# Performance work log

Measured on AMD Instinct MI355X. Metric: run time of the kernel, lower is better.

Reference implementation:

```python
import jax, jax.numpy as jnp
import numpy as np

N, F, H, T = 8192, 64, 64, 64   # nodes, fea_hid, gcn_hid, trans_hid
E = 262144                       # edges (avg degree 32)
S, K = 128, 128                  # subgraphs, subgraph size
NEG = 4                          # neg_num


def prelu(x, a):
    return jnp.where(x >= 0, x, a * x)


def setup_inputs() -> dict:
    key = jax.random.key(0)
    ks = jax.random.split(key, 20)
    inp = {}
    inp["feat"] = jax.random.normal(ks[0], (N, F), jnp.float32)
    inp["edge_src"] = jax.random.randint(ks[1], (E,), 0, N)
    inp["edge_dst"] = jax.random.randint(ks[2], (E,), 0, N)
    inp["edge_w"] = jax.random.uniform(ks[3], (E,), jnp.float32)   # normalized adj values
    inp["avg_w"] = jax.random.uniform(ks[4], (E,), jnp.float32)    # adj_avg values
    inp["neg_idx1"] = jax.random.randint(ks[5], (NEG, N), 0, N)
    inp["neg_idx2"] = jax.random.randint(ks[6], (NEG, N), 0, N)
    inp["a_subg_idx"] = jax.random.randint(ks[7], (S, K), 0, N)
    inp["n_subg_idx"] = jax.random.randint(ks[8], (S, K), 0, N)
    inp["a_lap"] = jax.random.normal(ks[9], (S, K, K), jnp.float32) * 0.1
    inp["n_lap"] = jax.random.normal(ks[10], (S, K, K), jnp.float32) * 0.1
    sc = lambda k, sh, d: jax.random.normal(k, sh, jnp.float32) / np.float32(np.sqrt(d))
    inp["W1"] = sc(ks[11], (F, H), F); inp["b1"] = jnp.zeros((H,), jnp.float32)
    inp["W2"] = sc(ks[12], (H, H), H); inp["b2"] = jnp.zeros((H,), jnp.float32)
    inp["Wq"] = sc(ks[13], (H, T), H); inp["bq"] = jnp.zeros((T,), jnp.float32)
    inp["Ws"] = sc(ks[14], (T, 1), T); inp["bs"] = jnp.zeros((1,), jnp.float32)
    inp["B1"] = sc(ks[15], (F, T), F); inp["bd1"] = jnp.zeros((), jnp.float32)
    inp["B2"] = sc(ks[16], (T, H), T); inp["bd2"] = jnp.zeros((), jnp.float32)
    inp["a1"] = jnp.full((), 0.25, jnp.float32)  # PReLU slopes
    inp["a2"] = jnp.full((), 0.25, jnp.float32)
    inp["aq"] = jnp.full((), 0.25, jnp.float32)
    return inp


def _agg(h, src, dst, w):
    # sparse matmul: (sparse adj) @ h via gather + segment_sum
    return jax.ops.segment_sum(w[:, None] * h[src], dst, num_segments=N)


def _forward(feat, edge_w, avg_w, a_lap, n_lap, W1, b1, W2, b2, Wq, bq, Ws, bs,
             B1, bd1, B2, bd2, a1, a2, aq,
             edge_src, edge_dst, neg_idx1, neg_idx2, a_subg_idx, n_subg_idx):
    # GCN 1: fc -> spmm -> +bias -> PReLU ; node_transemb = pre-propagation features
    h1 = feat @ W1                                             # [N,H]  node_transemb
    v1 = prelu(_agg(h1, edge_src, edge_dst, edge_w) + b1, a1)  # [N,H]
    # GCN 2
    h2 = v1 @ W2
    v2 = prelu(_agg(h2, edge_src, edge_dst, edge_w) + b2, a2)
    # transq + PReLU
    node_vec = prelu(v2 @ Wq + bq, aq)                          # [N,T]
    # AvgNeighbor on node_transemb
    node_neighbor = _agg(h1, edge_src, edge_dst, avg_w)         # [N,H]
    # Discriminator 1: bilinear(feat, node_vec); negatives shuffle feat
    p1 = jnp.einsum('nf,ft,nt->n', feat, B1, node_vec) + bd1    # [N]
    n1 = jnp.einsum('knf,ft,nt->kn', feat[neg_idx1], B1, node_vec) + bd1  # [NEG,N]
    # Discriminator 2: bilinear(node_vec, node_neighbor); negatives shuffle node_vec
    p2 = jnp.einsum('nt,th,nh->n', node_vec, B2, node_neighbor) + bd2
    n2 = jnp.einsum('knt,th,nh->kn', node_vec[neg_idx2], B2, node_neighbor) + bd2
    # MIL scores
    score = jax.nn.sigmoid(node_vec @ Ws + bs)[:, 0]            # [N]
    # batched subgraph losses (replaces ragged python loop)
    a_s = score[a_subg_idx]                                     # [S,K]
    n_s = score[n_subg_idx]                                     # [S,K]
    hom = (jnp.einsum('sk,skj,sj->s', a_s, a_lap, a_s)
           + jnp.einsum('sk,skj,sj->s', n_s, n_lap, n_s))       # [S]
    a_sort = -jnp.sort(-a_s, axis=1)                            # descending sort
    n_sort = -jnp.sort(-n_s, axis=1)
    # first position with value below the subgraph mean
    avg_idx = jnp.argmax(a_sort < jnp.mean(a_sort, axis=1, keepdims=True), axis=1)  # [S]
    a_at_avg = jnp.take_along_axis(a_sort, avg_idx[:, None], axis=1)[:, 0]
    ranking_loss = jnp.mean(jax.nn.relu(1.0 - a_sort[:, 0] + n_sort[:, 0]))
    ranking_inner_loss = jnp.mean(jax.nn.relu(1.0 - a_sort[:, 0] + a_at_avg))
    sp_loss = jnp.mean(jnp.sum(a_s, axis=1))
    hom_loss = jnp.sum(hom) / (2.0 * S)
    adj_rebuilt = jax.nn.sigmoid(node_vec @ node_vec.T)         # [N,N]
    return (ranking_loss, ranking_inner_loss, sp_loss, hom_loss, adj_rebuilt,
            p1, n1, p2, n2)


def reference(feat, edge_src, edge_dst, edge_w, avg_w, neg_idx1, neg_idx2,
              a_subg_idx, n_subg_idx, a_lap, n_lap,
              W1, b1, W2, b2, Wq, bq, Ws, bs, B1, bd1, B2, bd2, a1, a2, aq):
    return _forward(feat, edge_w, avg_w, a_lap, n_lap, W1, b1, W2, b2, Wq, bq, Ws, bs,
                    B1, bd1, B2, bd2, a1, a2, aq,
                    edge_src, edge_dst, neg_idx1, neg_idx2, a_subg_idx, n_subg_idx)
```

## Files before the change

### kernel.cpp

```cpp
#include <hip/hip_runtime.h>

#define Nn 8192
#define Ee 262144
#define NEGk 4

#define OFF_H1   0u
#define OFF_M1   524288u
#define OFF_V1   1048576u
#define OFF_NN   1572864u
#define OFF_H2   2097152u
#define OFF_V2   2621440u
#define OFF_NV   3145728u
#define OFF_M2   3670016u
#define OFF_SC   4194304u
#define OFF_CNT  4203008u
#define OFF_CUR  4211200u
#define OFF_RS   4219392u
#define OFF_ESRC 4227600u
#define OFF_EW   4489744u
#define OFF_EAW  4751888u
#define OFF_NVH  5014032u
#define OFF_NVL  5276176u
#define OFF_WT   5538320u

using short8 = __attribute__((ext_vector_type(8))) short;
using f32x4  = __attribute__((ext_vector_type(4))) float;

__device__ inline float wave_sum(float v){
  #pragma unroll
  for (int o = 32; o > 0; o >>= 1) v += __shfl_down(v, o, 64);
  return v;
}
__device__ inline float wave_max(float v){
  #pragma unroll
  for (int o = 32; o > 0; o >>= 1) v = fmaxf(v, __shfl_down(v, o, 64));
  return v;
}
__device__ inline unsigned short f2bf(float x){
  unsigned u = __float_as_uint(x);
  unsigned r = (u + 0x7FFFu + ((u >> 16) & 1u)) >> 16;
  return (unsigned short)r;
}
__device__ inline float bf2f(unsigned short h){ return __uint_as_float(((unsigned)h) << 16); }
__device__ inline float fsigmoid(float x){
  return __builtin_amdgcn_rcpf(1.f + __builtin_amdgcn_exp2f(-1.4426950408889634f * x));
}

__global__ __launch_bounds__(256) void prep_k(const float* __restrict__ W1, const float* __restrict__ B1,
    const float* __restrict__ W2, const float* __restrict__ Wq, const float* __restrict__ B2,
    float* __restrict__ Wt, int* __restrict__ cnt, int* __restrict__ cur, float* __restrict__ out4){
  int idx = blockIdx.x * 256 + threadIdx.x;
  if (idx < 20480){
    int m = idx >> 12, rc = idx & 4095;
    int k = rc >> 6, c = rc & 63;
    const float* src = (m == 0) ? W1 : (m == 1) ? B1 : (m == 2) ? W2 : (m == 3) ? Wq : B2;
    Wt[m * 4096 + c * 64 + k] = src[k * 64 + c];
  } else if (idx < 28672){
    cnt[idx - 20480] = 0;
  } else if (idx < 36864){
    cur[idx - 28672] = 0;
  } else if (idx < 36868){
    out4[idx - 36864] = 0.f;
  }
}

__global__ __launch_bounds__(256) void hist_k(const int* __restrict__ dst, int* __restrict__ cnt){
  int e = blockIdx.x * 256 + threadIdx.x;
  atomicAdd(&cnt[dst[e]], 1);
}

__global__ __launch_bounds__(256) void scan_k(const int* __restrict__ cnt, int* __restrict__ rs){
  __shared__ int part[256];
  int tid = threadIdx.x;
  int base = tid * 32;
  int local[32]; int s = 0;
  #pragma unroll
  for (int i = 0; i < 32; i++){ local[i] = s; s += cnt[base + i]; }
  part[tid] = s; __syncthreads();
  for (int off = 1; off < 256; off <<= 1){
    int v = (tid >= off) ? part[tid - off] : 0;
    __syncthreads();
    part[tid] += v;
    __syncthreads();
  }
  int ex = part[tid] - s;
  #pragma unroll
  for (int i = 0; i < 32; i++) rs[base + i] = ex + local[i];
  if (tid == 255) rs[Nn] = part[255];
}

__global__ __launch_bounds__(256) void scatter_k(const int* __restrict__ dst, const int* __restrict__ src,
    const float* __restrict__ ew, const float* __restrict__ aw,
    const int* __restrict__ rs, int* __restrict__ cur,
    int* __restrict__ cs, float* __restrict__ cw, float* __restrict__ caw){
  int e = blockIdx.x * 256 + threadIdx.x;
  int d = dst[e];
  int pos = atomicAdd(&cur[d], 1);
  int j = rs[d] + pos;
  cs[j] = src[e]; cw[j] = ew[e]; caw[j] = aw[e];
}

template<bool DUAL>
__global__ __launch_bounds__(256) void fc2_k(const float* __restrict__ X,
    const float* __restrict__ WtA, const float* __restrict__ WtB,
    float* __restrict__ Ya, float* __restrict__ Yb){
  __shared__ float As[32 * 68];
  int tid = threadIdx.x;
  int r0 = blockIdx.x * 32;
  for (int i = tid; i < 512; i += 256){
    int r = i >> 4, kq = (i & 15) << 2;
    *(float4*)(As + r * 68 + kq) = *(const float4*)(X + (r0 + r) * 64 + kq);
  }
  __syncthreads();
  int tx = tid & 63, wv = tid >> 6;
  float acca[8], accb[8];
  #pragma unroll
  for (int r = 0; r < 8; r++){ acca[r] = 0.f; accb[r] = 0.f; }
  const float* wpa = WtA + tx * 64;
  const float* wpb = DUAL ? (WtB + tx * 64) : WtA;
  #pragma unroll 4
  for (int kq = 0; kq < 64; kq += 4){
    float4 w = *(const float4*)(wpa + kq);
    float4 w2 = *(const float4*)(wpb + kq);
    #pragma unroll
    for (int r = 0; r < 8; r++){
      float4 a = *(const float4*)(As + (wv * 8 + r) * 68 + kq);
      acca[r] += a.x * w.x + a.y * w.y + a.z * w.z + a.w * w.w;
      if (DUAL) accb[r] += a.x * w2.x + a.y * w2.y + a.z * w2.z + a.w * w2.w;
    }
  }
  #pragma unroll
  for (int r = 0; r < 8; r++){
    int row = r0 + wv * 8 + r;
    Ya[row * 64 + tx] = acca[r];
    if (DUAL) Yb[row * 64 + tx] = accb[r];
  }
}

__global__ __launch_bounds__(256) void fcq_k(const float* __restrict__ X,
    const float* __restrict__ Wtq, const float* __restrict__ WtB2,
    const float* __restrict__ bias, const float* __restrict__ alpha,
    float* __restrict__ nv, float* __restrict__ M2,
    unsigned short* __restrict__ hi, unsigned short* __restrict__ lo){
  __shared__ float As[32 * 68];
  __shared__ float Ns[32 * 68];
  int tid = threadIdx.x;
  int r0 = blockIdx.x * 32;
  for (int i = tid; i < 512; i += 256){
    int r = i >> 4, kq = (i & 15) << 2;
    *(float4*)(As + r * 68 + kq) = *(const float4*)(X + (r0 + r) * 64 + kq);
  }
  __syncthreads();
  int tx = tid & 63, wv = tid >> 6;
  float acc[8];
  #pragma unroll
  for (int r = 0; r < 8; r++) acc[r] = 0.f;
  const float* wp = Wtq + tx * 64;
  #pragma unroll 4
  for (int kq = 0; kq < 64; kq += 4){
    float4 w = *(const float4*)(wp + kq);
    #pragma unroll
    for (int r = 0; r < 8; r++){
      float4 a = *(const float4*)(As + (wv * 8 + r) * 68 + kq);
      acc[r] += a.x * w.x + a.y * w.y + a.z * w.z + a.w * w.w;
    }
  }
  float al = alpha[0];
  float bi = bias[tx];
  #pragma unroll
  for (int r = 0; r < 8; r++){
    int row = r0 + wv * 8 + r;
    float x = acc[r] + bi;
    x = (x >= 0.f) ? x : al * x;
    nv[row * 64 + tx] = x;
    unsigned short h = f2bf(x);
    hi[row * 64 + tx] = h;
    lo[row * 64 + tx] = f2bf(x - bf2f(h));
    Ns[(wv * 8 + r) * 68 + tx] = x;
  }
  __syncthreads();
  float acc2[8];
  #pragma unroll
  for (int r = 0; r < 8; r++) acc2[r] = 0.f;
  const float* wp2 = WtB2 + tx * 64;
  #pragma unroll 4
  for (int kq = 0; kq < 64; kq += 4){
    float4 w = *(const float4*)(wp2 + kq);
    #pragma unroll
    for (int r = 0; r < 8; r++){
      float4 a = *(const float4*)(Ns + (wv * 8 + r) * 68 + kq);
      acc2[r] += a.x * w.x + a.y * w.y + a.z * w.z + a.w * w.w;
    }
  }
  #pragma unroll
  for (int r = 0; r < 8; r++){
    int row = r0 + wv * 8 + r;
    M2[row * 64 + tx] = acc2[r];
  }
}

template<bool DUAL>
__global__ __launch_bounds__(256) void agg_k(const float* __restrict__ h,
    const int* __restrict__ rs, const int* __restrict__ cs,
    const float* __restrict__ cw, const float* __restrict__ caw,
    const float* __restrict__ bias, const float* __restrict__ alpha,
    float* __restrict__ out1, float* __restrict__ out2){
  int node = (blockIdx.x << 2) + (threadIdx.x >> 6);
  int lane = threadIdx.x & 63;
  int s = rs[node], e = rs[node + 1];
  float acc = 0.f, acc2 = 0.f;
  int i = s;
  for (; i + 4 <= e; i += 4){
    int s0 = cs[i], s1 = cs[i+1], s2 = cs[i+2], s3 = cs[i+3];
    float w0 = cw[i], w1 = cw[i+1], w2 = cw[i+2], w3 = cw[i+3];
    float h0 = h[(s0 << 6) + lane];
    float h1v = h[(s1 << 6) + lane];
    float h2v = h[(s2 << 6) + lane];
    float h3 = h[(s3 << 6) + lane];
    acc += w0 * h0 + w1 * h1v + w2 * h2v + w3 * h3;
    if (DUAL){
      float a0 = caw[i], a1 = caw[i+1], a2 = caw[i+2], a3 = caw[i+3];
      acc2 += a0 * h0 + a1 * h1v + a2 * h2v + a3 * h3;
    }
  }
  for (; i < e; i++){
    int src = cs[i];
    float hv = h[(src << 6) + lane];
    acc += cw[i] * hv;
    if (DUAL) acc2 += caw[i] * hv;
  }
  float x = acc + bias[lane];
  float al = alpha[0];
  out1[(node << 6) + lane] = (x >= 0.f) ? x : al * x;
  if (DUAL) out2[(node << 6) + lane] = acc2;
}

__global__ __launch_bounds__(256) void dotsneg_k(const float* __restrict__ nv,
    const float* __restrict__ M1, const float* __restrict__ M2, const float* __restrict__ nn,
    const float* __restrict__ Wsv, const float* __restrict__ bs,
    const float* __restrict__ bd1, const float* __restrict__ bd2,
    const int* __restrict__ neg1, const int* __restrict__ neg2,
    float* __restrict__ p1, float* __restrict__ p2, float* __restrict__ score,
    float* __restrict__ n1, float* __restrict__ n2){
  int b = blockIdx.x;
  int wv = threadIdx.x >> 6, t = threadIdx.x & 63;
  if (b < (Nn >> 2)){
    int node = (b << 2) + wv;
    float v = nv[(node << 6) + t];
    float s1 = wave_sum(M1[(node << 6) + t] * v);
    float s2 = wave_sum(M2[(node << 6) + t] * nn[(node << 6) + t]);
    float s3 = wave_sum(v * Wsv[t]);
    if (t == 0){
      p1[node] = s1 + bd1[0];
      p2[node] = s2 + bd2[0];
      score[node] = fsigmoid(s3 + bs[0]);
    }
  } else {
    int gid = ((b - (Nn >> 2)) << 2) + wv;
    int n = gid & (Nn - 1);
    int i1 = neg1[gid], i2 = neg2[gid];
    float d1 = wave_sum(M1[(i1 << 6) + t] * nv[(n << 6) + t]);
    float d2 = wave_sum(M2[(i2 << 6) + t] * nn[(n << 6) + t]);
    if (t == 0){ n1[gid] = d1 + bd1[0]; n2[gid] = d2 + bd2[0]; }
  }
}

__global__ __launch_bounds__(256) void subg_k(const float* __restrict__ score,
    const int* __restrict__ aidx, const int* __restrict__ nidx,
    const float* __restrict__ alap, const float* __restrict__ nlap,
    float* __restrict__ out){
  __shared__ float as_[128], ns_[128];
  __shared__ float pya[256], pyn[256];
  __shared__ float red[4];
  int s = blockIdx.x, t = threadIdx.x;
  int r = t >> 1, half = t & 1;
  if (t < 128){
    as_[t] = score[aidx[s * 128 + t]];
    ns_[t] = score[nidx[s * 128 + t]];
  }
  __syncthreads();
  const float* la = alap + (size_t)s * 16384 + r * 128 + half * 64;
  const float* ln = nlap + (size_t)s * 16384 + r * 128 + half * 64;
  float ya = 0.f, yn = 0.f;
  #pragma unroll 4
  for (int j = 0; j < 64; j += 4){
    int jj = half * 64 + j;
    float4 wa = *(const float4*)(la + j);
    ya += wa.x * as_[jj] + wa.y * as_[jj + 1] + wa.z * as_[jj + 2] + wa.w * as_[jj + 3];
    float4 wn = *(const float4*)(ln + j);
    yn += wn.x * ns_[jj] + wn.y * ns_[jj + 1] + wn.z * ns_[jj + 2] + wn.w * ns_[jj + 3];
  }
  pya[t] = ya; pyn[t] = yn;
  __syncthreads();
  int wid = t >> 6, lane = t & 63;
  float av = 0.f, nvv = 0.f, hom = 0.f;
  bool act = (t < 128);
  if (act){
    av = as_[t]; nvv = ns_[t];
    hom = av * (pya[2 * t] + pya[2 * t + 1]) + nvv * (pyn[2 * t] + pyn[2 * t + 1]);
  }
  float w;
  w = wave_sum(act ? av : 0.f); if (lane == 0) red[wid] = w; __syncthreads();
  float sumA = red[0] + red[1] + red[2] + red[3]; __syncthreads();
  w = wave_sum(hom); if (lane == 0) red[wid] = w; __syncthreads();
  float homS = red[0] + red[1] + red[2] + red[3]; __syncthreads();
  w = wave_max(act ? av : -3.0e38f); if (lane == 0) red[wid] = w; __syncthreads();
  float maxA = fmaxf(fmaxf(red[0], red[1]), fmaxf(red[2], red[3])); __syncthreads();
  w = wave_max(act ? nvv : -3.0e38f); if (lane == 0) red[wid] = w; __syncthreads();
  float maxN = fmaxf(fmaxf(red[0], red[1]), fmaxf(red[2], red[3])); __syncthreads();
  float mean = sumA * (1.f / 128.f);
  float below = (act && av < mean) ? av : -3.0e38f;
  w = wave_max(below); if (lane == 0) red[wid] = w; __syncthreads();
  float mb = fmaxf(fmaxf(red[0], red[1]), fmaxf(red[2], red[3]));
  float a_at_avg = (mb < -1.0e37f) ? maxA : mb;
  if (t == 0){
    atomicAdd(out + 0, fmaxf(0.f, 1.f - maxA + maxN) * (1.f / 128.f));
    atomicAdd(out + 1, fmaxf(0.f, 1.f - maxA + a_at_avg) * (1.f / 128.f));
    atomicAdd(out + 2, sumA * (1.f / 128.f));
    atomicAdd(out + 3, homS * (1.f / 256.f));
  }
}

__global__ __launch_bounds__(256) void adj_mfma_k(const unsigned short* __restrict__ hi,
    const unsigned short* __restrict__ lo, float* __restrict__ C){
  __shared__ __align__(16) float st[4][16 * 68];
  int tid = threadIdx.x;
  int wave = tid >> 6, lane = tid & 63;
  int quad = lane >> 4, m = lane & 15;
  int rowBase = (blockIdx.y << 7) + ((wave >> 1) << 6);
  int colBase = (blockIdx.x << 7) + ((wave & 1) << 6);

  f32x4 acc[4][4];
  #pragma unroll
  for (int i = 0; i < 4; i++)
    #pragma unroll
    for (int j = 0; j < 4; j++) acc[i][j] = (f32x4){0.f, 0.f, 0.f, 0.f};

  const unsigned short* Ah = hi + ((rowBase + m) << 6) + (quad << 3);
  const unsigned short* Al = lo + ((rowBase + m) << 6) + (quad << 3);
  const unsigned short* Bh = hi + ((colBase + m) << 6) + (quad << 3);
  const unsigned short* Bl = lo + ((colBase + m) << 6) + (quad << 3);

  #pragma unroll
  for (int h = 0; h < 2; h++){
    int ko = h << 5;
    short8 ah[4], al[4], bh[4], bl[4];
    #pragma unroll
    for (int i = 0; i < 4; i++){
      ah[i] = *(const short8*)(Ah + (i << 10) + ko);
      al[i] = *(const short8*)(Al + (i << 10) + ko);
      bh[i] = *(const short8*)(Bh + (i << 10) + ko);
      bl[i] = *(const short8*)(Bl + (i << 10) + ko);
    }
    #pragma unroll
    for (int i = 0; i < 4; i++)
      #pragma unroll
      for (int j = 0; j < 4; j++){
        acc[i][j] = __builtin_amdgcn_mfma_f32_16x16x32_bf16(ah[i], bh[j], acc[i][j], 0, 0, 0);
        acc[i][j] = __builtin_amdgcn_mfma_f32_16x16x32_bf16(ah[i], bl[j], acc[i][j], 0, 0, 0);
        acc[i][j] = __builtin_amdgcn_mfma_f32_16x16x32_bf16(al[i], bh[j], acc[i][j], 0, 0, 0);
      }
  }

  int rr = lane >> 4;
  int c4 = lane & 15;
  float* S = st[wave];
  #pragma unroll
  for (int i = 0; i < 4; i++){
    #pragma unroll
    for (int j = 0; j < 4; j++)
      #pragma unroll
      for (int r = 0; r < 4; r++)
        S[((quad << 2) + r) * 68 + (j << 4) + m] = acc[i][j][r];
    #pragma unroll
    for (int t = 0; t < 4; t++){
      int row_l = rr + (t << 2);
      f32x4 v = *(const f32x4*)(S + row_l * 68 + (c4 << 2));
      f32x4 o;
      o[0] = fsigmoid(v[0]);
      o[1] = fsigmoid(v[1]);
      o[2] = fsigmoid(v[2]);
      o[3] = fsigmoid(v[3]);
      size_t row = (size_t)(rowBase + (i << 4) + row_l);
      __builtin_nontemporal_store(o, (f32x4*)(C + row * Nn + colBase + (c4 << 2)));
    }
  }
}

extern "C" void kernel_launch(void* const* d_in, const int* in_sizes, int n_in,
                              void* d_out, int out_size, void* d_ws, size_t ws_size,
                              hipStream_t stream) {
  const float* feat  = (const float*)d_in[0];
  const int*   esrc  = (const int*)d_in[1];
  const int*   edst  = (const int*)d_in[2];
  const float* ewv   = (const float*)d_in[3];
  const float* eawv  = (const float*)d_in[4];
  const int*   neg1  = (const int*)d_in[5];
  const int*   neg2  = (const int*)d_in[6];
  const int*   aidx  = (const int*)d_in[7];
  const int*   nidx  = (const int*)d_in[8];
  const float* alap  = (const float*)d_in[9];
  const float* nlap  = (const float*)d_in[10];
  const float* W1    = (const float*)d_in[11];
  const float* b1    = (const float*)d_in[12];
  const float* W2    = (const float*)d_in[13];
  const float* b2    = (const float*)d_in[14];
  const float* Wq    = (const float*)d_in[15];
  const float* bq    = (const float*)d_in[16];
  const float* Wsv   = (const float*)d_in[17];
  const float* bs    = (const float*)d_in[18];
  const float* B1    = (const float*)d_in[19];
  const float* bd1   = (const float*)d_in[20];
  const float* B2    = (const float*)d_in[21];
  const float* bd2   = (const float*)d_in[22];
  const float* a1    = (const float*)d_in[23];
  const float* a2    = (const float*)d_in[24];
  const float* aq    = (const float*)d_in[25];

  float* ws  = (float*)d_ws;
  float* h1  = ws + OFF_H1;
  float* M1  = ws + OFF_M1;
  float* v1  = ws + OFF_V1;
  float* nn  = ws + OFF_NN;
  float* h2  = ws + OFF_H2;
  float* v2  = ws + OFF_V2;
  float* nv  = ws + OFF_NV;
  float* M2  = ws + OFF_M2;
  float* sc  = ws + OFF_SC;
  int*   cnt = (int*)(ws + OFF_CNT);
  int*   cur = (int*)(ws + OFF_CUR);
  int*   rs  = (int*)(ws + OFF_RS);
  int*   cs  = (int*)(ws + OFF_ESRC);
  float* cw  = ws + OFF_EW;
  float* caw = ws + OFF_EAW;
  unsigned short* nvh = (unsigned short*)(ws + OFF_NVH);
  unsigned short* nvl = (unsigned short*)(ws + OFF_NVL);
  float* Wt  = ws + OFF_WT;
  float* Wt1 = Wt;           float* WtB1 = Wt + 4096;
  float* Wt2 = Wt + 8192;    float* Wtq  = Wt + 12288;
  float* WtB2 = Wt + 16384;

  float* out = (float*)d_out;
  float* adj = out + 4;
  float* p1  = adj + (size_t)Nn * Nn;
  float* n1o = p1 + Nn;
  float* p2  = n1o + NEGk * Nn;
  float* n2o = p2 + Nn;

  prep_k<<<145, 256, 0, stream>>>(W1, B1, W2, Wq, B2, Wt, cnt, cur, out);
  hist_k<<<Ee / 256, 256, 0, stream>>>(edst, cnt);
  scan_k<<<1, 256, 0, stream>>>(cnt, rs);
  scatter_k<<<Ee / 256, 256, 0, stream>>>(edst, esrc, ewv, eawv, rs, cur, cs, cw, caw);

  fc2_k<true ><<<Nn / 32, 256, 0, stream>>>(feat, Wt1, WtB1, h1, M1);
  agg_k<true ><<<Nn / 4, 256, 0, stream>>>(h1, rs, cs, cw, caw, b1, a1, v1, nn);
  fc2_k<false><<<Nn / 32, 256, 0, stream>>>(v1, Wt2, nullptr, h2, nullptr);
  agg_k<false><<<Nn / 4, 256, 0, stream>>>(h2, rs, cs, cw, caw, b2, a2, v2, nullptr);
  fcq_k<<<Nn / 32, 256, 0, stream>>>(v2, Wtq, WtB2, bq, aq, nv, M2, nvh, nvl);

  dotsneg_k<<<(Nn / 4) + (NEGk * Nn / 4), 256, 0, stream>>>(nv, M1, M2, nn, Wsv, bs, bd1, bd2,
                                                            neg1, neg2, p1, p2, sc, n1o, n2o);

  subg_k<<<128, 256, 0, stream>>>(sc, aidx, nidx, alap, nlap, out);

  adj_mfma_k<<<dim3(Nn / 128, Nn / 128), 256, 0, stream>>>(nvh, nvl, adj);
}
```

Baseline: 495.5 us.

## Restructure adjacency MFMA kernel into row-strip tiles with wide contiguous stores

The adjacency-rebuild GEMM changes from 128x128 block tiles to blocks that own a 16-row strip. Each of two waves sweeps 2048 columns in 256-column chunks, keeping the A fragments in registers and streaming B from global memory. Output rows are now staged so each wave writes 1 KB contiguous runs, and the nontemporal store hint is replaced by a normal store. The aim is more coalesced writes of the large N×N output. In exchange, B operands are reloaded far more often, since each block rereads half of the hi/lo matrix, and the grid drops to 1024 blocks of 2 waves with less parallel occupancy.

```diff
diff --git a/kernel.cpp b/kernel.cpp
--- a/kernel.cpp
+++ b/kernel.cpp
@@ -321,68 +321,57 @@
   }
 }
 
-__global__ __launch_bounds__(256) void adj_mfma_k(const unsigned short* __restrict__ hi,
+__global__ __launch_bounds__(128) void adj_mfma_k(const unsigned short* __restrict__ hi,
     const unsigned short* __restrict__ lo, float* __restrict__ C){
-  __shared__ __align__(16) float st[4][16 * 68];
+  __shared__ __align__(16) float st[2][16 * 260];
   int tid = threadIdx.x;
   int wave = tid >> 6, lane = tid & 63;
   int quad = lane >> 4, m = lane & 15;
-  int rowBase = (blockIdx.y << 7) + ((wave >> 1) << 6);
-  int colBase = (blockIdx.x << 7) + ((wave & 1) << 6);
-
-  f32x4 acc[4][4];
-  #pragma unroll
-  for (int i = 0; i < 4; i++)
-    #pragma unroll
-    for (int j = 0; j < 4; j++) acc[i][j] = (f32x4){0.f, 0.f, 0.f, 0.f};
-
-  const unsigned short* Ah = hi + ((rowBase + m) << 6) + (quad << 3);
-  const unsigned short* Al = lo + ((rowBase + m) << 6) + (quad << 3);
-  const unsigned short* Bh = hi + ((colBase + m) << 6) + (quad << 3);
-  const unsigned short* Bl = lo + ((colBase + m) << 6) + (quad << 3);
-
-  #pragma unroll
-  for (int h = 0; h < 2; h++){
-    int ko = h << 5;
-    short8 ah[4], al[4], bh[4], bl[4];
-    #pragma unroll
-    for (int i = 0; i < 4; i++){
-      ah[i] = *(const short8*)(Ah + (i << 10) + ko);
-      al[i] = *(const short8*)(Al + (i << 10) + ko);
-      bh[i] = *(const short8*)(Bh + (i << 10) + ko);
-      bl[i] = *(const short8*)(Bl + (i << 10) + ko);
-    }
-    #pragma unroll
-    for (int i = 0; i < 4; i++)
-      #pragma unroll
-      for (int j = 0; j < 4; j++){
-        acc[i][j] = __builtin_amdgcn_mfma_f32_16x16x32_bf16(ah[i], bh[j], acc[i][j], 0, 0, 0);
-        acc[i][j] = __builtin_amdgcn_mfma_f32_16x16x32_bf16(ah[i], bl[j], acc[i][j], 0, 0, 0);
-        acc[i][j] = __builtin_amdgcn_mfma_f32_16x16x32_bf16(al[i], bh[j], acc[i][j], 0, 0, 0);
-      }
-  }
-
-  int rr = lane >> 4;
-  int c4 = lane & 15;
+  int R0 = blockIdx.y << 4;
+  int colBase = (blockIdx.x << 12) + (wave << 11);
+
+  short8 ah[2], al[2];
+  #pragma unroll
+  for (int kh = 0; kh < 2; kh++){
+    ah[kh] = *(const short8*)(hi + ((R0 + m) << 6) + (kh << 5) + (quad << 3));
+    al[kh] = *(const short8*)(lo + ((R0 + m) << 6) + (kh << 5) + (quad << 3));
+  }
+
   float* S = st[wave];
-  #pragma unroll
-  for (int i = 0; i < 4; i++){
-    #pragma unroll
-    for (int j = 0; j < 4; j++)
+  for (int it = 0; it < 8; it++){
+    int Ci = colBase + (it << 8);
+    f32x4 acc[16];
+    #pragma unroll
+    for (int j = 0; j < 16; j++) acc[j] = (f32x4){0.f, 0.f, 0.f, 0.f};
+    #pragma unroll
+    for (int j = 0; j < 16; j++){
+      const unsigned short* bph = hi + ((Ci + (j << 4) + m) << 6) + (quad << 3);
+      const unsigned short* bpl = lo + ((Ci + (j << 4) + m) << 6) + (quad << 3);
+      short8 bh0 = *(const short8*)(bph);
+      short8 bh1 = *(const short8*)(bph + 32);
+      short8 bl0 = *(const short8*)(bpl);
+      short8 bl1 = *(const short8*)(bpl + 32);
+      acc[j] = __builtin_amdgcn_mfma_f32_16x16x32_bf16(ah[0], bh0, acc[j], 0, 0, 0);
+      acc[j] = __builtin_amdgcn_mfma_f32_16x16x32_bf16(ah[0], bl0, acc[j], 0, 0, 0);
+      acc[j] = __builtin_amdgcn_mfma_f32_16x16x32_bf16(al[0], bh0, acc[j], 0, 0, 0);
+      acc[j] = __builtin_amdgcn_mfma_f32_16x16x32_bf16(ah[1], bh1, acc[j], 0, 0, 0);
+      acc[j] = __builtin_amdgcn_mfma_f32_16x16x32_bf16(ah[1], bl1, acc[j], 0, 0, 0);
+      acc[j] = __builtin_amdgcn_mfma_f32_16x16x32_bf16(al[1], bh1, acc[j], 0, 0, 0);
+    }
+    #pragma unroll
+    for (int j = 0; j < 16; j++)
       #pragma unroll
       for (int r = 0; r < 4; r++)
-        S[((quad << 2) + r) * 68 + (j << 4) + m] = acc[i][j][r];
-    #pragma unroll
-    for (int t = 0; t < 4; t++){
-      int row_l = rr + (t << 2);
-      f32x4 v = *(const f32x4*)(S + row_l * 68 + (c4 << 2));
+        S[((quad << 2) + r) * 260 + (j << 4) + m] = acc[j][r];
+    #pragma unroll
+    for (int r16 = 0; r16 < 16; r16++){
+      f32x4 v = *(const f32x4*)(S + r16 * 260 + (lane << 2));
       f32x4 o;
       o[0] = fsigmoid(v[0]);
       o[1] = fsigmoid(v[1]);
       o[2] = fsigmoid(v[2]);
       o[3] = fsigmoid(v[3]);
-      size_t row = (size_t)(rowBase + (i << 4) + row_l);
-      __builtin_nontemporal_store(o, (f32x4*)(C + row * Nn + colBase + (c4 << 2)));
+      *(f32x4*)(C + (size_t)(R0 + r16) * Nn + Ci + (lane << 2)) = o;
     }
   }
 }
@@ -463,5 +452,5 @@
 
   subg_k<<<128, 256, 0, stream>>>(sc, aidx, nidx, alap, nlap, out);
 
-  adj_mfma_k<<<dim3(Nn / 128, Nn / 128), 256, 0, stream>>>(nvh, nvl, adj);
-}
+  adj_mfma_k<<<dim3(2, 512), 128, 0, stream>>>(nvh, nvl, adj);
+}
```

Result: slower. 543.0 us (+9.6%).
